# Kernel tuning notes

Hardware: AMD Instinct MI355X
Metric: run time of the kernel (lower is better)

## Reference

```python
import jax, jax.numpy as jnp
import numpy as np
from jax import lax

B, C, H, W = 16, 256, 56, 56
MID = 16  # SE: max(C//16, 4)
EPS = 1e-5


def _bn(x, g, b, m, v):
    # inference-mode BatchNorm2d folded to per-channel scale/shift
    s = g * lax.rsqrt(v + EPS)
    return x * s[None, :, None, None] + (b - m * s)[None, :, None, None]


def _dw(x, w, ph, pw):
    # depthwise conv, NCHW, kernel w: [C,1,kh,kw]
    return lax.conv_general_dilated(
        x, w, window_strides=(1, 1), padding=[(ph, ph), (pw, pw)],
        dimension_numbers=('NCHW', 'OIHW', 'NCHW'), feature_group_count=C)


def _pw(x, w):
    # 1x1 conv, w: [O,C,1,1]
    return jnp.einsum('bchw,oc->bohw', x, w[:, :, 0, 0])


def _se(x, w1, b1, w2, b2):
    s = x.mean(axis=(2, 3))                      # [B,C] squeeze
    s = jax.nn.relu(s @ w1.T + b1)               # [B,MID]
    s = jax.nn.sigmoid(s @ w2.T + b2)            # [B,C]
    return x * s[:, :, None, None]


def setup_inputs() -> dict:
    key = jax.random.key(0)
    ks = jax.random.split(key, 32)
    rn = lambda i, shape, sc=0.05: jax.random.normal(ks[i], shape, jnp.float32) * sc
    ru = lambda i, shape: jax.random.uniform(ks[i], shape, jnp.float32)
    return {
        'x': rn(0, (B, C, H, W), 1.0),
        'pw1_w': rn(1, (C, C, 1, 1)),
        'xy3_w': rn(2, (C, 1, 3, 3)), 'xy5_w': rn(3, (C, 1, 5, 5)),
        'bnxy_g': ru(4, (C,)), 'bnxy_b': rn(5, (C,)), 'bnxy_m': rn(6, (C,)), 'bnxy_v': ru(7, (C,)),
        'xz3_w': rn(8, (C, 1, 1, 3)), 'xz5_w': rn(9, (C, 1, 1, 5)),
        'bnxz_g': ru(10, (C,)), 'bnxz_b': rn(11, (C,)), 'bnxz_m': rn(12, (C,)), 'bnxz_v': ru(13, (C,)),
        'yz3_w': rn(14, (C, 1, 3, 1)), 'yz5_w': rn(15, (C, 1, 5, 1)),
        'bnyz_g': ru(16, (C,)), 'bnyz_b': rn(17, (C,)), 'bnyz_m': rn(18, (C,)), 'bnyz_v': ru(19, (C,)),
        'alpha': jnp.full((1, C, 1, 1), 0.5, jnp.float32),
        'beta': jnp.full((1, C, 1, 1), 0.5, jnp.float32),
        'pw2_w': rn(20, (C, C, 1, 1)),
        'bn2_g': ru(21, (C,)), 'bn2_b': rn(22, (C,)), 'bn2_m': rn(23, (C,)), 'bn2_v': ru(24, (C,)),
        'fc1_w': rn(25, (MID, C)), 'fc1_b': rn(26, (MID,)),
        'fc2_w': rn(27, (C, MID)), 'fc2_b': rn(28, (C,)),
    }


def reference(x, pw1_w, xy3_w, xy5_w, bnxy_g, bnxy_b, bnxy_m, bnxy_v,
              xz3_w, xz5_w, bnxz_g, bnxz_b, bnxz_m, bnxz_v,
              yz3_w, yz5_w, bnyz_g, bnyz_b, bnyz_m, bnyz_v,
              alpha, beta, pw2_w, bn2_g, bn2_b, bn2_m, bn2_v,
              fc1_w, fc1_b, fc2_w, fc2_b):
    # Pw1: 1x1 conv, no BN / no act
    out = _pw(x, pw1_w)
    # MS_TOP (stride=1 -> pool is identity)
    # [B] xy branch: DW 3x3 + DW 5x5 -> BN -> ReLU
    f_xy = jax.nn.relu(_bn(_dw(out, xy3_w, 1, 1) + _dw(out, xy5_w, 2, 2),
                           bnxy_g, bnxy_b, bnxy_m, bnxy_v))
    # [A] xz branch: per-row depthwise Conv1d along W == depthwise (1,k) 2D conv
    f_xz = jax.nn.relu(_bn(_dw(out, xz3_w, 0, 1) + _dw(out, xz5_w, 0, 2),
                           bnxz_g, bnxz_b, bnxz_m, bnxz_v))
    # [A] yz branch: per-column depthwise Conv1d along H == depthwise (k,1) 2D conv
    f_yz = jax.nn.relu(_bn(_dw(out, yz3_w, 1, 0) + _dw(out, yz5_w, 2, 0),
                           bnyz_g, bnyz_b, bnyz_m, bnyz_v))
    # [C] learnable-gate fusion
    gate = jax.nn.sigmoid(alpha * f_xz + beta * f_yz)
    top = jax.nn.relu(f_xy * gate)
    # Pw2: 1x1 conv -> BN -> ReLU
    out2 = jax.nn.relu(_bn(_pw(top, pw2_w), bn2_g, bn2_b, bn2_m, bn2_v))
    # SE channel attention
    out2 = _se(out2, fc1_w, fc1_b, fc2_w, fc2_b)
    # DropPath is identity at inference; shortcut is identity (stride=1, in==out)
    return out2 + x
```

## Files before the change

kernel.cpp:

```cpp
#include <hip/hip_runtime.h>
#include <math.h>

typedef __bf16 bf16;
typedef __bf16 bf16x8 __attribute__((ext_vector_type(8)));
typedef __bf16 bf16x4 __attribute__((ext_vector_type(4)));
typedef float f32x4 __attribute__((ext_vector_type(4)));

#define CC 256
#define BB 16
#define HH 56
#define WW 56
#define HWSZ 3136
#define EPS 1e-5f

#define OFF_SCALE 0
#define OFF_SUMS  16384
#define OFF_WBF1  32768
#define OFF_WBF2  163840
#define OFF_WDW   294912
#define OFF_BNC   312832
#define OFF_OUT2  321024

__global__ __launch_bounds__(256) void precast(
    const float* __restrict__ w1, const float* __restrict__ w2,
    const float* __restrict__ xy3, const float* __restrict__ xy5,
    const float* __restrict__ xz3, const float* __restrict__ xz5,
    const float* __restrict__ yz3, const float* __restrict__ yz5,
    const float* __restrict__ gxy, const float* __restrict__ bxy,
    const float* __restrict__ mxy, const float* __restrict__ vxy,
    const float* __restrict__ gxz, const float* __restrict__ bxz,
    const float* __restrict__ mxz, const float* __restrict__ vxz,
    const float* __restrict__ gyz, const float* __restrict__ byz,
    const float* __restrict__ myz, const float* __restrict__ vyz,
    const float* __restrict__ alpha, const float* __restrict__ beta,
    bf16* __restrict__ wbf1, bf16* __restrict__ wbf2,
    bf16* __restrict__ wdw, float* __restrict__ bnc,
    float* __restrict__ sums)
{
    const int blk = blockIdx.x, t = threadIdx.x;
    if (blk < 128) {
        int i = blk * 512 + t * 2;
        wbf1[i] = (bf16)w1[i]; wbf1[i + 1] = (bf16)w1[i + 1];
    } else if (blk < 256) {
        int i = (blk - 128) * 512 + t * 2;
        wbf2[i] = (bf16)w2[i]; wbf2[i + 1] = (bf16)w2[i + 1];
    } else {
        const int c = t;
#pragma unroll
        for (int dh = 0; dh < 5; ++dh)
#pragma unroll
            for (int dw = 0; dw < 5; ++dw) {
                float v = xy5[c * 25 + dh * 5 + dw];
                if (dh >= 1 && dh <= 3 && dw >= 1 && dw <= 3)
                    v += xy3[c * 9 + (dh - 1) * 3 + (dw - 1)];
                wdw[(dh * 5 + dw) * CC + c] = (bf16)v;
            }
#pragma unroll
        for (int d = 0; d < 5; ++d) {
            float v = xz5[c * 5 + d];
            if (d >= 1 && d <= 3) v += xz3[c * 3 + d - 1];
            wdw[(25 + d) * CC + c] = (bf16)v;
            float u = yz5[c * 5 + d];
            if (d >= 1 && d <= 3) u += yz3[c * 3 + d - 1];
            wdw[(30 + d) * CC + c] = (bf16)u;
        }
        float s;
        s = gxy[c] * rsqrtf(vxy[c] + EPS); bnc[0*CC+c] = s; bnc[1*CC+c] = bxy[c] - mxy[c]*s;
        s = gxz[c] * rsqrtf(vxz[c] + EPS); bnc[2*CC+c] = s; bnc[3*CC+c] = bxz[c] - mxz[c]*s;
        s = gyz[c] * rsqrtf(vyz[c] + EPS); bnc[4*CC+c] = s; bnc[5*CC+c] = byz[c] - myz[c]*s;
        bnc[6*CC+c] = alpha[c]; bnc[7*CC+c] = beta[c];
        for (int i = t; i < BB * CC; i += 256) sums[i] = 0.f;
    }
}

__global__ __launch_bounds__(256) void pw_gemm1(
    const float* __restrict__ in, const bf16* __restrict__ wbf,
    bf16* __restrict__ mid)
{
    __shared__ __align__(16) bf16 XT[64][264];
    const int hw0 = blockIdx.x * 64;
    const int b   = blockIdx.y;
    const int t   = threadIdx.x;

    {
        const int hwg = (t & 15) * 4;
        const int cig = (t >> 4) * 4;
        const float* base = in + (size_t)b * CC * HWSZ + hw0 + hwg;
#pragma unroll
        for (int pass = 0; pass < 4; ++pass) {
            const int ci0 = pass * 64 + cig;
            f32x4 v[4];
#pragma unroll
            for (int i = 0; i < 4; ++i)
                v[i] = *(const f32x4*)(base + (size_t)(ci0 + i) * HWSZ);
#pragma unroll
            for (int j = 0; j < 4; ++j) {
                bf16x4 r = {(bf16)v[0][j], (bf16)v[1][j], (bf16)v[2][j], (bf16)v[3][j]};
                *(bf16x4*)(&XT[hwg + j][ci0]) = r;
            }
        }
    }
    __syncthreads();

    const int lane = t & 63, wv = t >> 6;
    const int q = lane >> 4, n = lane & 15;
    const int co_w = wv * 64;

    const bf16* wp[4];
#pragma unroll
    for (int cf = 0; cf < 4; ++cf)
        wp[cf] = wbf + (size_t)(co_w + cf * 16 + n) * CC + q * 8;

    f32x4 acc[4][4] = {};
#pragma unroll
    for (int kk = 0; kk < 8; ++kk) {
        bf16x8 aq[4], bq[4];
#pragma unroll
        for (int cf = 0; cf < 4; ++cf) aq[cf] = *(const bf16x8*)(wp[cf] + kk * 32);
#pragma unroll
        for (int hf = 0; hf < 4; ++hf)
            bq[hf] = *(const bf16x8*)(&XT[hf * 16 + n][kk * 32 + q * 8]);
#pragma unroll
        for (int cf = 0; cf < 4; ++cf)
#pragma unroll
            for (int hf = 0; hf < 4; ++hf)
                acc[cf][hf] = __builtin_amdgcn_mfma_f32_16x16x32_bf16(
                    aq[cf], bq[hf], acc[cf][hf], 0, 0, 0);
    }

    bf16* ob = mid + ((size_t)b * HWSZ + hw0) * CC;
#pragma unroll
    for (int cf = 0; cf < 4; ++cf) {
        const int co4 = co_w + cf * 16 + q * 4;
#pragma unroll
        for (int hf = 0; hf < 4; ++hf) {
            bf16x4 r = {(bf16)acc[cf][hf][0], (bf16)acc[cf][hf][1],
                        (bf16)acc[cf][hf][2], (bf16)acc[cf][hf][3]};
            *(bf16x4*)(ob + (size_t)(hf * 16 + n) * CC + co4) = r;
        }
    }
}

__global__ __launch_bounds__(256) void dwfuse(
    const bf16* __restrict__ mid, const bf16* __restrict__ wdw,
    const float* __restrict__ bnc, bf16* __restrict__ top)
{
    __shared__ __align__(16) bf16  lw[35 * 256];
    __shared__ __align__(16) float lbn[8 * 256];
    const int t = threadIdx.x;
    for (int i = t; i < 35 * 256; i += 256) lw[i] = wdw[i];
    for (int i = t; i < 8 * 256; i += 256) lbn[i] = bnc[i];
    __syncthreads();

    const int w  = blockIdx.x * 8 + (t >> 5);
    const int h0 = blockIdx.y * 2;
    const int b  = blockIdx.z;
    const int c0 = (t & 31) * 8;
    const size_t plane = (size_t)b * HWSZ;

    float axy[2][8] = {}, axz[2][8] = {}, ayz[2][8] = {};
#pragma unroll
    for (int dhh = 0; dhh < 6; ++dhh) {
        const int hh = h0 - 2 + dhh;
        if ((unsigned)hh >= (unsigned)HH) continue;
#pragma unroll
        for (int dw = 0; dw < 5; ++dw) {
            const int ww = w + dw - 2;
            if ((unsigned)ww >= (unsigned)WW) continue;
            bf16x8 v = *(const bf16x8*)(mid + ((plane + hh * WW + ww) * CC + c0));
            float fv[8];
#pragma unroll
            for (int j = 0; j < 8; ++j) fv[j] = (float)v[j];
#pragma unroll
            for (int p = 0; p < 2; ++p) {
                const int dh = dhh - p;
                if (dh < 0 || dh > 4) continue;
                bf16x8 wc = *(const bf16x8*)(&lw[(dh * 5 + dw) * 256 + c0]);
#pragma unroll
                for (int j = 0; j < 8; ++j) axy[p][j] += (float)wc[j] * fv[j];
                if (dh == 2) {
                    bf16x8 wz = *(const bf16x8*)(&lw[(25 + dw) * 256 + c0]);
#pragma unroll
                    for (int j = 0; j < 8; ++j) axz[p][j] += (float)wz[j] * fv[j];
                }
                if (dw == 2) {
                    bf16x8 wy = *(const bf16x8*)(&lw[(30 + dh) * 256 + c0]);
#pragma unroll
                    for (int j = 0; j < 8; ++j) ayz[p][j] += (float)wy[j] * fv[j];
                }
            }
        }
    }

#pragma unroll
    for (int p = 0; p < 2; ++p) {
        bf16x8 r;
#pragma unroll
        for (int j = 0; j < 8; ++j) {
            const int c = c0 + j;
            const float fxy = fmaxf(axy[p][j] * lbn[c]         + lbn[256 + c], 0.f);
            const float fxz = fmaxf(axz[p][j] * lbn[2*256 + c] + lbn[3*256 + c], 0.f);
            const float fyz = fmaxf(ayz[p][j] * lbn[4*256 + c] + lbn[5*256 + c], 0.f);
            const float z   = lbn[6*256 + c] * fxz + lbn[7*256 + c] * fyz;
            const float g   = 1.f / (1.f + expf(-z));
            r[j] = (bf16)fmaxf(fxy * g, 0.f);
        }
        *(bf16x8*)(top + ((plane + (h0 + p) * WW + w) * CC + c0)) = r;
    }
}

__global__ __launch_bounds__(256) void pw_gemm2(
    const bf16* __restrict__ top, const bf16* __restrict__ wbf,
    const float* __restrict__ g2, const float* __restrict__ b2,
    const float* __restrict__ m2, const float* __restrict__ v2,
    bf16* __restrict__ out2, float* __restrict__ sums)
{
    __shared__ __align__(16) bf16 XT[64][264];
    const int hw0 = blockIdx.x * 64;
    const int b   = blockIdx.y;
    const int t   = threadIdx.x;

    {
        const int hw_r = t >> 2;
        const int k0   = (t & 3) * 64;
        const bf16* src = top + ((size_t)b * HWSZ + hw0 + hw_r) * CC + k0;
#pragma unroll
        for (int j = 0; j < 8; ++j)
            *(bf16x8*)(&XT[hw_r][k0 + j * 8]) = *(const bf16x8*)(src + j * 8);
    }
    __syncthreads();

    const int lane = t & 63, wv = t >> 6;
    const int q = lane >> 4, n = lane & 15;
    const int co_w = wv * 64;

    const bf16* wp[4];
#pragma unroll
    for (int cf = 0; cf < 4; ++cf)
        wp[cf] = wbf + (size_t)(co_w + cf * 16 + n) * CC + q * 8;

    f32x4 acc[4][4] = {};
#pragma unroll
    for (int kk = 0; kk < 8; ++kk) {
        bf16x8 aq[4], bq[4];
#pragma unroll
        for (int cf = 0; cf < 4; ++cf) aq[cf] = *(const bf16x8*)(wp[cf] + kk * 32);
#pragma unroll
        for (int hf = 0; hf < 4; ++hf)
            bq[hf] = *(const bf16x8*)(&XT[hf * 16 + n][kk * 32 + q * 8]);
#pragma unroll
        for (int cf = 0; cf < 4; ++cf)
#pragma unroll
            for (int hf = 0; hf < 4; ++hf)
                acc[cf][hf] = __builtin_amdgcn_mfma_f32_16x16x32_bf16(
                    aq[cf], bq[hf], acc[cf][hf], 0, 0, 0);
    }

    bf16* ob = out2 + ((size_t)b * HWSZ + hw0) * CC;
#pragma unroll
    for (int cf = 0; cf < 4; ++cf) {
        const int co4 = co_w + cf * 16 + q * 4;
        f32x4 g = *(const f32x4*)(g2 + co4);
        f32x4 bb = *(const f32x4*)(b2 + co4);
        f32x4 mm = *(const f32x4*)(m2 + co4);
        f32x4 vv = *(const f32x4*)(v2 + co4);
        f32x4 sc, sh;
#pragma unroll
        for (int r = 0; r < 4; ++r) {
            sc[r] = g[r] * rsqrtf(vv[r] + EPS);
            sh[r] = bb[r] - mm[r] * sc[r];
        }
        f32x4 rs = {};
#pragma unroll
        for (int hf = 0; hf < 4; ++hf) {
            bf16x4 r4;
#pragma unroll
            for (int r = 0; r < 4; ++r) {
                float v = fmaxf(acc[cf][hf][r] * sc[r] + sh[r], 0.f);
                rs[r] += v;
                r4[r] = (bf16)v;
            }
            *(bf16x4*)(ob + (size_t)(hf * 16 + n) * CC + co4) = r4;
        }
#pragma unroll
        for (int msk = 1; msk < 16; msk <<= 1)
#pragma unroll
            for (int r = 0; r < 4; ++r) rs[r] += __shfl_xor(rs[r], msk);
        if (n == 0) {
#pragma unroll
            for (int r = 0; r < 4; ++r)
                atomicAdd(&sums[b * CC + co4 + r], rs[r]);
        }
    }
}

__global__ __launch_bounds__(256) void se_fc(
    const float* __restrict__ sums,
    const float* __restrict__ w1, const float* __restrict__ b1,
    const float* __restrict__ w2, const float* __restrict__ b2,
    float* __restrict__ scale)
{
    __shared__ float mean[256];
    __shared__ float hid[16];
    const int b = blockIdx.x, tid = threadIdx.x;
    mean[tid] = sums[b * CC + tid] * (1.f / (float)HWSZ);
    __syncthreads();
    if (tid < 16) {
        float h = b1[tid];
        for (int cd = 0; cd < 256; ++cd) h += w1[tid * 256 + cd] * mean[cd];
        hid[tid] = fmaxf(h, 0.f);
    }
    __syncthreads();
    float v = b2[tid];
#pragma unroll
    for (int md = 0; md < 16; ++md) v += w2[tid * 16 + md] * hid[md];
    scale[b * CC + tid] = 1.f / (1.f + expf(-v));
}

__global__ __launch_bounds__(256) void se_apply(
    const bf16* __restrict__ out2, const float* __restrict__ x,
    const float* __restrict__ scale, float* __restrict__ out)
{
    __shared__ float TT[64 * 68];
    const int hw0 = blockIdx.x * 64;
    const int c0  = blockIdx.y * 64;
    const int b   = blockIdx.z;
    const int t   = threadIdx.x;

    {
        const int hw_r = t >> 2;
        const int coff = (t & 3) * 16;
        const bf16* p = out2 + ((size_t)b * HWSZ + hw0 + hw_r) * CC + c0 + coff;
        bf16x8 u0 = *(const bf16x8*)(p);
        bf16x8 u1 = *(const bf16x8*)(p + 8);
        const float* sp = scale + b * CC + c0 + coff;
        f32x4 s0 = *(const f32x4*)(sp), s1 = *(const f32x4*)(sp + 4);
        f32x4 s2 = *(const f32x4*)(sp + 8), s3 = *(const f32x4*)(sp + 12);
#pragma unroll
        for (int j = 0; j < 4; ++j) {
            TT[(coff + j)      * 68 + hw_r] = (float)u0[j]     * s0[j];
            TT[(coff + 4 + j)  * 68 + hw_r] = (float)u0[4 + j] * s1[j];
            TT[(coff + 8 + j)  * 68 + hw_r] = (float)u1[j]     * s2[j];
            TT[(coff + 12 + j) * 68 + hw_r] = (float)u1[4 + j] * s3[j];
        }
    }
    __syncthreads();
    {
        const int c_r   = t >> 2;
        const int hwoff = (t & 3) * 16;
        const size_t go = ((size_t)b * CC + c0 + c_r) * HWSZ + hw0 + hwoff;
#pragma unroll
        for (int v = 0; v < 4; ++v) {
            f32x4 tv = *(const f32x4*)(&TT[c_r * 68 + hwoff + v * 4]);
            f32x4 xv = *(const f32x4*)(x + go + v * 4);
#pragma unroll
            for (int j = 0; j < 4; ++j) tv[j] += xv[j];
            *(f32x4*)(out + go + v * 4) = tv;
        }
    }
}

extern "C" void kernel_launch(void* const* d_in, const int* in_sizes, int n_in,
                              void* d_out, int out_size, void* d_ws, size_t ws_size,
                              hipStream_t stream)
{
    const float* x      = (const float*)d_in[0];
    const float* pw1_w  = (const float*)d_in[1];
    const float* xy3_w  = (const float*)d_in[2];
    const float* xy5_w  = (const float*)d_in[3];
    const float* bnxy_g = (const float*)d_in[4];
    const float* bnxy_b = (const float*)d_in[5];
    const float* bnxy_m = (const float*)d_in[6];
    const float* bnxy_v = (const float*)d_in[7];
    const float* xz3_w  = (const float*)d_in[8];
    const float* xz5_w  = (const float*)d_in[9];
    const float* bnxz_g = (const float*)d_in[10];
    const float* bnxz_b = (const float*)d_in[11];
    const float* bnxz_m = (const float*)d_in[12];
    const float* bnxz_v = (const float*)d_in[13];
    const float* yz3_w  = (const float*)d_in[14];
    const float* yz5_w  = (const float*)d_in[15];
    const float* bnyz_g = (const float*)d_in[16];
    const float* bnyz_b = (const float*)d_in[17];
    const float* bnyz_m = (const float*)d_in[18];
    const float* bnyz_v = (const float*)d_in[19];
    const float* alpha  = (const float*)d_in[20];
    const float* beta   = (const float*)d_in[21];
    const float* pw2_w  = (const float*)d_in[22];
    const float* bn2_g  = (const float*)d_in[23];
    const float* bn2_b  = (const float*)d_in[24];
    const float* bn2_m  = (const float*)d_in[25];
    const float* bn2_v  = (const float*)d_in[26];
    const float* fc1_w  = (const float*)d_in[27];
    const float* fc1_b  = (const float*)d_in[28];
    const float* fc2_w  = (const float*)d_in[29];
    const float* fc2_b  = (const float*)d_in[30];

    const size_t NEL = (size_t)BB * CC * HWSZ;
    char* ws = (char*)d_ws;
    float* scale = (float*)(ws + OFF_SCALE);
    float* sums  = (float*)(ws + OFF_SUMS);
    bf16*  wbf1  = (bf16*) (ws + OFF_WBF1);
    bf16*  wbf2  = (bf16*) (ws + OFF_WBF2);
    bf16*  wdw   = (bf16*) (ws + OFF_WDW);
    float* bnc   = (float*)(ws + OFF_BNC);
    bf16*  out2  = (bf16*) (ws + OFF_OUT2);
    bf16*  mid   = (bf16*)d_out;
    bf16*  top   = (bf16*)d_out + NEL;

    precast<<<257, 256, 0, stream>>>(pw1_w, pw2_w,
        xy3_w, xy5_w, xz3_w, xz5_w, yz3_w, yz5_w,
        bnxy_g, bnxy_b, bnxy_m, bnxy_v,
        bnxz_g, bnxz_b, bnxz_m, bnxz_v,
        bnyz_g, bnyz_b, bnyz_m, bnyz_v,
        alpha, beta, wbf1, wbf2, wdw, bnc, sums);

    pw_gemm1<<<dim3(49, 16), 256, 0, stream>>>(x, wbf1, mid);
    dwfuse<<<dim3(7, 28, 16), 256, 0, stream>>>(mid, wdw, bnc, top);
    pw_gemm2<<<dim3(49, 16), 256, 0, stream>>>(top, wbf2, bn2_g, bn2_b,
                                               bn2_m, bn2_v, out2, sums);
    se_fc<<<BB, 256, 0, stream>>>(sums, fc1_w, fc1_b, fc2_w, fc2_b, scale);
    se_apply<<<dim3(49, 4, 16), 256, 0, stream>>>(out2, x, scale, (float*)d_out);
}
```

Baseline: 321.3 us.

## Prefetch GEMM weights into registers before staging, duplicate depthwise weights in LDS

Both pointwise GEMM kernels now load all of their A-operand weight fragments into registers before the activation tile is staged into LDS, so global weight latency overlaps with the staging and barrier. They also gain a minimum-blocks-per-CU launch bound. The depthwise fused kernel stores its weights in LDS duplicated across a 512-wide stride, which is meant to spread LDS bank accesses across the two half-waves. It also reads BN constants straight from global memory into registers instead of from LDS, shrinking shared memory. The cost is higher register pressure from 32 bf16x8 weight fragments per thread, which under the occupancy bound could cause spills.

New measurement: 295.1 us. -8.1%, faster.

```diff
diff --git a/kernel.cpp b/kernel.cpp
--- a/kernel.cpp
+++ b/kernel.cpp
@@ -73,7 +73,7 @@
     }
 }
 
-__global__ __launch_bounds__(256) void pw_gemm1(
+__global__ __launch_bounds__(256, 2) void pw_gemm1(
     const float* __restrict__ in, const bf16* __restrict__ wbf,
     bf16* __restrict__ mid)
 {
@@ -81,6 +81,18 @@
     const int hw0 = blockIdx.x * 64;
     const int b   = blockIdx.y;
     const int t   = threadIdx.x;
+    const int lane = t & 63, wv = t >> 6;
+    const int q = lane >> 4, n = lane & 15;
+    const int co_w = wv * 64;
+
+    bf16x8 aq[4][8];
+#pragma unroll
+    for (int cf = 0; cf < 4; ++cf) {
+        const bf16* wp = wbf + (size_t)(co_w + cf * 16 + n) * CC + q * 8;
+#pragma unroll
+        for (int kk = 0; kk < 8; ++kk)
+            aq[cf][kk] = *(const bf16x8*)(wp + kk * 32);
+    }
 
     {
         const int hwg = (t & 15) * 4;
@@ -102,21 +114,10 @@
     }
     __syncthreads();
 
-    const int lane = t & 63, wv = t >> 6;
-    const int q = lane >> 4, n = lane & 15;
-    const int co_w = wv * 64;
-
-    const bf16* wp[4];
-#pragma unroll
-    for (int cf = 0; cf < 4; ++cf)
-        wp[cf] = wbf + (size_t)(co_w + cf * 16 + n) * CC + q * 8;
-
     f32x4 acc[4][4] = {};
 #pragma unroll
     for (int kk = 0; kk < 8; ++kk) {
-        bf16x8 aq[4], bq[4];
-#pragma unroll
-        for (int cf = 0; cf < 4; ++cf) aq[cf] = *(const bf16x8*)(wp[cf] + kk * 32);
+        bf16x8 bq[4];
 #pragma unroll
         for (int hf = 0; hf < 4; ++hf)
             bq[hf] = *(const bf16x8*)(&XT[hf * 16 + n][kk * 32 + q * 8]);
@@ -125,7 +126,7 @@
 #pragma unroll
             for (int hf = 0; hf < 4; ++hf)
                 acc[cf][hf] = __builtin_amdgcn_mfma_f32_16x16x32_bf16(
-                    aq[cf], bq[hf], acc[cf][hf], 0, 0, 0);
+                    aq[cf][kk], bq[hf], acc[cf][hf], 0, 0, 0);
     }
 
     bf16* ob = mid + ((size_t)b * HWSZ + hw0) * CC;
@@ -145,18 +146,21 @@
     const bf16* __restrict__ mid, const bf16* __restrict__ wdw,
     const float* __restrict__ bnc, bf16* __restrict__ top)
 {
-    __shared__ __align__(16) bf16  lw[35 * 256];
-    __shared__ __align__(16) float lbn[8 * 256];
+    __shared__ __align__(16) bf16 lw2[35 * 512];
     const int t = threadIdx.x;
-    for (int i = t; i < 35 * 256; i += 256) lw[i] = wdw[i];
-    for (int i = t; i < 8 * 256; i += 256) lbn[i] = bnc[i];
+    for (int idx = t; idx < 35 * 64; idx += 256) {
+        const int tap = idx >> 6, slot = idx & 63;
+        *(bf16x8*)(&lw2[tap * 512 + slot * 8]) =
+            *(const bf16x8*)(wdw + tap * 256 + (slot & 31) * 8);
+    }
     __syncthreads();
 
     const int w  = blockIdx.x * 8 + (t >> 5);
     const int h0 = blockIdx.y * 2;
-    const int b  = blockIdx.z;
+    const int bb = blockIdx.z;
     const int c0 = (t & 31) * 8;
-    const size_t plane = (size_t)b * HWSZ;
+    const int ls = (t & 63) * 8;
+    const size_t plane = (size_t)bb * HWSZ;
 
     float axy[2][8] = {}, axz[2][8] = {}, ayz[2][8] = {};
 #pragma unroll
@@ -175,16 +179,16 @@
             for (int p = 0; p < 2; ++p) {
                 const int dh = dhh - p;
                 if (dh < 0 || dh > 4) continue;
-                bf16x8 wc = *(const bf16x8*)(&lw[(dh * 5 + dw) * 256 + c0]);
+                bf16x8 wc = *(const bf16x8*)(&lw2[(dh * 5 + dw) * 512 + ls]);
 #pragma unroll
                 for (int j = 0; j < 8; ++j) axy[p][j] += (float)wc[j] * fv[j];
                 if (dh == 2) {
-                    bf16x8 wz = *(const bf16x8*)(&lw[(25 + dw) * 256 + c0]);
+                    bf16x8 wz = *(const bf16x8*)(&lw2[(25 + dw) * 512 + ls]);
 #pragma unroll
                     for (int j = 0; j < 8; ++j) axz[p][j] += (float)wz[j] * fv[j];
                 }
                 if (dw == 2) {
-                    bf16x8 wy = *(const bf16x8*)(&lw[(30 + dh) * 256 + c0]);
+                    bf16x8 wy = *(const bf16x8*)(&lw2[(30 + dh) * 512 + ls]);
 #pragma unroll
                     for (int j = 0; j < 8; ++j) ayz[p][j] += (float)wy[j] * fv[j];
                 }
@@ -192,16 +196,24 @@
         }
     }
 
+    float bnv[8][8];
+#pragma unroll
+    for (int k = 0; k < 8; ++k) {
+        f32x4 a0 = *(const f32x4*)(bnc + k * CC + c0);
+        f32x4 a1 = *(const f32x4*)(bnc + k * CC + c0 + 4);
+#pragma unroll
+        for (int j = 0; j < 4; ++j) { bnv[k][j] = a0[j]; bnv[k][4 + j] = a1[j]; }
+    }
+
 #pragma unroll
     for (int p = 0; p < 2; ++p) {
         bf16x8 r;
 #pragma unroll
         for (int j = 0; j < 8; ++j) {
-            const int c = c0 + j;
-            const float fxy = fmaxf(axy[p][j] * lbn[c]         + lbn[256 + c], 0.f);
-            const float fxz = fmaxf(axz[p][j] * lbn[2*256 + c] + lbn[3*256 + c], 0.f);
-            const float fyz = fmaxf(ayz[p][j] * lbn[4*256 + c] + lbn[5*256 + c], 0.f);
-            const float z   = lbn[6*256 + c] * fxz + lbn[7*256 + c] * fyz;
+            const float fxy = fmaxf(axy[p][j] * bnv[0][j] + bnv[1][j], 0.f);
+            const float fxz = fmaxf(axz[p][j] * bnv[2][j] + bnv[3][j], 0.f);
+            const float fyz = fmaxf(ayz[p][j] * bnv[4][j] + bnv[5][j], 0.f);
+            const float z   = bnv[6][j] * fxz + bnv[7][j] * fyz;
             const float g   = 1.f / (1.f + expf(-z));
             r[j] = (bf16)fmaxf(fxy * g, 0.f);
         }
@@ -209,7 +221,7 @@
     }
 }
 
-__global__ __launch_bounds__(256) void pw_gemm2(
+__global__ __launch_bounds__(256, 2) void pw_gemm2(
     const bf16* __restrict__ top, const bf16* __restrict__ wbf,
     const float* __restrict__ g2, const float* __restrict__ b2,
     const float* __restrict__ m2, const float* __restrict__ v2,
@@ -219,6 +231,18 @@
     const int hw0 = blockIdx.x * 64;
     const int b   = blockIdx.y;
     const int t   = threadIdx.x;
+    const int lane = t & 63, wv = t >> 6;
+    const int q = lane >> 4, n = lane & 15;
+    const int co_w = wv * 64;
+
+    bf16x8 aq[4][8];
+#pragma unroll
+    for (int cf = 0; cf < 4; ++cf) {
+        const bf16* wp = wbf + (size_t)(co_w + cf * 16 + n) * CC + q * 8;
+#pragma unroll
+        for (int kk = 0; kk < 8; ++kk)
+            aq[cf][kk] = *(const bf16x8*)(wp + kk * 32);
+    }
 
     {
         const int hw_r = t >> 2;
@@ -230,21 +254,10 @@
     }
     __syncthreads();
 
-    const int lane = t & 63, wv = t >> 6;
-    const int q = lane >> 4, n = lane & 15;
-    const int co_w = wv * 64;
-
-    const bf16* wp[4];
-#pragma unroll
-    for (int cf = 0; cf < 4; ++cf)
-        wp[cf] = wbf + (size_t)(co_w + cf * 16 + n) * CC + q * 8;
-
     f32x4 acc[4][4] = {};
 #pragma unroll
     for (int kk = 0; kk < 8; ++kk) {
-        bf16x8 aq[4], bq[4];
-#pragma unroll
-        for (int cf = 0; cf < 4; ++cf) aq[cf] = *(const bf16x8*)(wp[cf] + kk * 32);
+        bf16x8 bq[4];
 #pragma unroll
         for (int hf = 0; hf < 4; ++hf)
             bq[hf] = *(const bf16x8*)(&XT[hf * 16 + n][kk * 32 + q * 8]);
@@ -253,7 +266,7 @@
 #pragma unroll
             for (int hf = 0; hf < 4; ++hf)
                 acc[cf][hf] = __builtin_amdgcn_mfma_f32_16x16x32_bf16(
-                    aq[cf], bq[hf], acc[cf][hf], 0, 0, 0);
+                    aq[cf][kk], bq[hf], acc[cf][hf], 0, 0, 0);
     }
 
     bf16* ob = out2 + ((size_t)b * HWSZ + hw0) * CC;
```
